# Optimization experiments

Hardware: AMD Instinct MI355X
Metric: run time of the kernel (lower is better)

Reference implementation:

```python
import jax, jax.numpy as jnp
from jax import lax
import numpy as np

B, N, NPOINT, NSAMPLE = 4, 8192, 1024, 32
RADIUS = 0.2
EPS = 1e-5
C_IN = 16
MLP_DIMS = [(3 + C_IN, 64), (64, 64), (64, 128)]


def setup_inputs() -> dict:
    key = jax.random.key(0)
    ks = jax.random.split(key, 16)
    inp = {
        "xyz": jax.random.uniform(ks[0], (B, N, 3), dtype=jnp.float32),
        "points": jax.random.normal(ks[1], (B, N, C_IN), dtype=jnp.float32),
    }
    for i, (cin, cout) in enumerate(MLP_DIMS, 1):
        inp[f"w{i}"] = jax.random.normal(ks[1 + i], (cout, cin), dtype=jnp.float32) / np.sqrt(cin)
        inp[f"b{i}"] = jnp.zeros((cout,), jnp.float32)
        inp[f"g{i}"] = jnp.ones((cout,), jnp.float32)
        inp[f"be{i}"] = jnp.zeros((cout,), jnp.float32)
    return inp


def fps(xyz, npoint):
    # Farthest point sampling; sequential by nature -> lax.scan over npoint steps.
    # Deterministic start at index 0 (torch version uses a random start).
    b, n, _ = xyz.shape
    def step(carry, _):
        dist, far = carry
        centroid = jnp.take_along_axis(xyz, far[:, None, None], axis=1)  # [B,1,3]
        d = jnp.sum((xyz - centroid) ** 2, -1)                            # [B,N]
        dist = jnp.minimum(dist, d)
        return (dist, jnp.argmax(dist, -1).astype(jnp.int32)), far
    init = (jnp.full((b, n), 1e10, xyz.dtype), jnp.zeros((b,), jnp.int32))
    _, idxs = lax.scan(step, init, None, length=npoint)
    return jnp.transpose(idxs)  # [B, npoint]


def gather2(pts, idx):  # pts [B,N,C], idx [B,S] -> [B,S,C]
    return jnp.take_along_axis(pts, idx[..., None], axis=1)


def gather3(pts, idx):  # pts [B,N,C], idx [B,S,K] -> [B,S,K,C]
    b, s, k = idx.shape
    out = jnp.take_along_axis(pts, idx.reshape(b, s * k)[..., None], axis=1)
    return out.reshape(b, s, k, pts.shape[-1])


def ball_query(radius, nsample, xyz, new_xyz):
    n = xyz.shape[1]
    # [B,S,N] pairwise squared distances (the memory-bound hot spot)
    sqr = jnp.sum((new_xyz[:, :, None, :] - xyz[:, None, :, :]) ** 2, -1)
    gidx = jnp.where(sqr > radius * radius, n, jnp.arange(n, dtype=jnp.int32))
    gidx = jnp.sort(gidx, axis=-1)[:, :, :nsample]
    first = gidx[:, :, :1]
    return jnp.where(gidx == n, first, gidx)


def mlp_layer(x, w, b, g, be):
    # 1x1 Conv2d + BatchNorm2d (train mode: batch stats over B,S,K) + ReLU
    y = jnp.einsum('bskc,oc->bsko', x, w) + b
    mu = jnp.mean(y, axis=(0, 1, 2))
    var = jnp.var(y, axis=(0, 1, 2))
    y = (y - mu) * (g * lax.rsqrt(var + EPS)) + be
    return jax.nn.relu(y)


def reference(xyz, points, w1, b1, g1, be1, w2, b2, g2, be2, w3, b3, g3, be3):
    fps_idx = fps(xyz, NPOINT)                       # [B,S]
    new_xyz = gather2(xyz, fps_idx)                  # [B,S,3]
    idx = ball_query(RADIUS, NSAMPLE, xyz, new_xyz)  # [B,S,K]
    grouped_xyz_norm = gather3(xyz, idx) - new_xyz[:, :, None, :]  # [B,S,K,3]
    grouped_points = gather3(points, idx)            # [B,S,K,C]
    feat = jnp.concatenate([grouped_xyz_norm, grouped_points], -1)  # [B,S,K,3+C]
    feat = mlp_layer(feat, w1, b1, g1, be1)
    feat = mlp_layer(feat, w2, b2, g2, be2)
    feat = mlp_layer(feat, w3, b3, g3, be3)
    new_points = jnp.max(feat, axis=2)               # max-pool over neighbors -> [B,S,128]
    return new_xyz, new_points
```

## Files before the change

kernel.cpp:

```cpp
#include <hip/hip_runtime.h>

#define NB 4
#define NP 8192
#define NS 1024
#define NK 32
#define CNT_ALL 131072.0f

typedef float v2f __attribute__((ext_vector_type(2)));
typedef unsigned long long u64;

#define AGENT __HIP_MEMORY_SCOPE_AGENT

template <int CTRL>
__device__ __forceinline__ unsigned dpp_max_u32(unsigned m)
{
    unsigned o = (unsigned)__builtin_amdgcn_update_dpp((int)m, (int)m, CTRL, 0xF, 0xF, false);
    return (o > m) ? o : m;
}

template <int CTRL>
__device__ __forceinline__ u64 dpp_max_u64(u64 k)
{
    unsigned lo = (unsigned)k, hi = (unsigned)(k >> 32);
    unsigned olo = (unsigned)__builtin_amdgcn_update_dpp((int)lo, (int)lo, CTRL, 0xF, 0xF, false);
    unsigned ohi = (unsigned)__builtin_amdgcn_update_dpp((int)hi, (int)hi, CTRL, 0xF, 0xF, false);
    u64 o = ((u64)ohi << 32) | (u64)olo;
    return (o > k) ? o : k;
}

__global__ __launch_bounds__(512, 1) void k1_kernel(
    const float* __restrict__ xyz, const float* __restrict__ pts,
    float* __restrict__ newxyz,
    const float* __restrict__ w1, const float* __restrict__ b1,
    float* __restrict__ y1, float* __restrict__ st, unsigned* __restrict__ prog)
{
    __shared__ __align__(16) char smem[98432];
    const int tid = threadIdx.x;
    const int lane = tid & 63;
    const int wv = tid >> 6;

    if (blockIdx.x < NB) {
#pragma clang fp contract(off)
        float* s_px = (float*)smem;
        float* s_py = (float*)(smem + 32768);
        float* s_pz = (float*)(smem + 65536);
        u64*   s_kv = (u64*)(smem + 98304);
        const int b = blockIdx.x;
        const float* xb = xyz + (size_t)b * NP * 3;

#pragma unroll
        for (int k = 0; k < 16; ++k) {
            const int i = k * 512 + tid;
            s_px[i] = xb[3 * i + 0];
            s_py[i] = xb[3 * i + 1];
            s_pz[i] = xb[3 * i + 2];
        }
        __syncthreads();

        v2f px[8], py[8], pz[8], dist[8];
        const int base = tid << 4;
#pragma unroll
        for (int m = 0; m < 8; ++m) {
            const int p0 = base + 2 * m;
            px[m] = v2f{s_px[p0], s_px[p0 + 1]};
            py[m] = v2f{s_py[p0], s_py[p0 + 1]};
            pz[m] = v2f{s_pz[p0], s_pz[p0 + 1]};
            dist[m] = v2f{1e10f, 1e10f};
        }
        float cx = s_px[0], cy = s_py[0], cz = s_pz[0];
        float* ob = newxyz + (size_t)b * NS * 3;

        for (int it = 0; it < NS; ++it) {
            if (tid == 0) {
                __hip_atomic_store(&prog[b], (unsigned)it, __ATOMIC_RELAXED, AGENT);
                __hip_atomic_store(&ob[it * 3 + 0], cx, __ATOMIC_RELAXED, AGENT);
                __hip_atomic_store(&ob[it * 3 + 1], cy, __ATOMIC_RELAXED, AGENT);
                __hip_atomic_store(&ob[it * 3 + 2], cz, __ATOMIC_RELAXED, AGENT);
            }
            const v2f cxx = v2f{cx, cx}, cyy = v2f{cy, cy}, czz = v2f{cz, cz};
            v2f bdv = v2f{-1.0f, -1.0f};
#pragma unroll
            for (int m = 0; m < 8; ++m) {
                v2f dx = px[m] - cxx, dy = py[m] - cyy, dz = pz[m] - czz;
                v2f d = __builtin_elementwise_fma(dz, dz,
                            __builtin_elementwise_fma(dy, dy, dx * dx));
                v2f dj = __builtin_elementwise_min(dist[m], d);
                dist[m] = dj;
                bdv = __builtin_elementwise_max(bdv, dj);
            }
            const float bd = fmaxf(bdv.x, bdv.y);
            const unsigned ub = __float_as_uint(bd);
            unsigned m0 = dpp_max_u32<0xB1>(ub);
            m0 = dpp_max_u32<0x4E>(m0);
            m0 = dpp_max_u32<0x141>(m0);
            m0 = dpp_max_u32<0x140>(m0);
            m0 = dpp_max_u32<0x142>(m0);
            m0 = dpp_max_u32<0x143>(m0);
            const unsigned maxbits = (unsigned)__builtin_amdgcn_readlane((int)m0, 63);
            const float bdw = __uint_as_float(maxbits);
            int jb = 0;
#pragma unroll
            for (int m = 7; m >= 0; --m) {
                jb = (dist[m].y == bdw) ? (2 * m + 1) : jb;
                jb = (dist[m].x == bdw) ? (2 * m) : jb;
            }
            const u64 bm = __ballot(ub == maxbits);
            const int srclane = __ffsll(bm) - 1;
            const int wbi = __builtin_amdgcn_readlane(base + jb, srclane);
            if (lane == 0)
                s_kv[(it & 1) * 8 + wv] = ((u64)maxbits << 32) | (unsigned)(NP - 1 - wbi);
            __syncthreads();
            u64 kv = s_kv[(it & 1) * 8 + (lane & 7)];
            kv = dpp_max_u64<0xB1>(kv);
            kv = dpp_max_u64<0x4E>(kv);
            kv = dpp_max_u64<0x141>(kv);
            const int fi = NP - 1 - (int)(unsigned)(kv & 0xFFFFFFFFull);
            cx = s_px[fi]; cy = s_py[fi]; cz = s_pz[fi];
        }
        if (tid == 0)
            __hip_atomic_store(&prog[b], (unsigned)NS, __ATOMIC_RELAXED, AGENT);
        return;
    }

    int*   s_ball = (int*)smem;
    float* s_cent = (float*)(smem + 1024);
    float* s_feat = (float*)(smem + 1152);
    float* s_ps   = (float*)(smem + 1152 + 20480);
    float* s_pq   = s_ps + 512;

    const int abk = blockIdx.x - NB;
    const int b = abk >> 5;
    const int s0 = (abk & 31) * 32;
    const float* xb = xyz + (size_t)b * NP * 3;
    const float rr = (float)(0.2 * 0.2);

    const int c = tid & 63, rg = tid >> 6;
    float wvr[20];
#pragma unroll
    for (int j = 0; j < 19; ++j) wvr[j] = w1[c * 19 + j];
    wvr[19] = 0.f;
    const float bs = b1[c];
    float sa = 0.f, qa = 0.f;

    for (int chunk = 0; chunk < 4; ++chunk) {
        const int sl = s0 + chunk * 8;
        if (tid == 0) {
            while ((int)__hip_atomic_load(&prog[b], __ATOMIC_RELAXED, AGENT) < sl + 8)
                __builtin_amdgcn_s_sleep(4);
        }
        __syncthreads();
        {
            const int sg = (b << 10) + sl + wv;
            float cxv, cyv, czv;
            if (lane == 0) {
                cxv = __hip_atomic_load(&newxyz[sg * 3 + 0], __ATOMIC_RELAXED, AGENT);
                cyv = __hip_atomic_load(&newxyz[sg * 3 + 1], __ATOMIC_RELAXED, AGENT);
                czv = __hip_atomic_load(&newxyz[sg * 3 + 2], __ATOMIC_RELAXED, AGENT);
                s_cent[wv * 4 + 0] = cxv;
                s_cent[wv * 4 + 1] = cyv;
                s_cent[wv * 4 + 2] = czv;
            }
            cxv = __shfl(cxv, 0); cyv = __shfl(cyv, 0); czv = __shfl(czv, 0);
            int cnt = 0;
            for (int bse = 0; bse < NP && cnt < NK; bse += 64) {
                const int p = bse + lane;
                float dx = xb[p * 3 + 0] - cxv;
                float dy = xb[p * 3 + 1] - cyv;
                float dz = xb[p * 3 + 2] - czv;
                float d = __fadd_rn(__fadd_rn(__fmul_rn(dx, dx), __fmul_rn(dy, dy)),
                                    __fmul_rn(dz, dz));
                bool in = (d <= rr);
                u64 mask = __ballot(in);
                int before = __popcll(mask & ((1ull << lane) - 1ull));
                int pos = cnt + before;
                if (in && pos < NK) s_ball[wv * NK + pos] = p;
                cnt += (int)__popcll(mask);
            }
            cnt = min(cnt, NK);
            const int v0 = s_ball[wv * NK];
            if (lane < NK && lane >= cnt) s_ball[wv * NK + lane] = v0;
        }
        __syncthreads();
        if (tid < 256) {
            const int lg = tid >> 5, k = tid & 31;
            const int id = s_ball[lg * NK + k];
            const float* pp = xyz + ((size_t)b * NP + id) * 3;
            float* f = s_feat + tid * 20;
            f[0] = pp[0] - s_cent[lg * 4 + 0];
            f[1] = pp[1] - s_cent[lg * 4 + 1];
            f[2] = pp[2] - s_cent[lg * 4 + 2];
            const float4* q4 = (const float4*)(pts + ((size_t)b * NP + id) * 16);
#pragma unroll
            for (int i = 0; i < 4; ++i) {
                float4 v = q4[i];
                f[3 + 4 * i + 0] = v.x; f[3 + 4 * i + 1] = v.y;
                f[3 + 4 * i + 2] = v.z; f[3 + 4 * i + 3] = v.w;
            }
            f[19] = 0.f;
        }
        __syncthreads();
        const size_t rowbase = (size_t)abk * 1024 + (size_t)chunk * 256;
        for (int r = 0; r < 32; ++r) {
            const int row = rg * 32 + r;
            const float4* f4 = (const float4*)(s_feat + row * 20);
            float acc = bs;
#pragma unroll
            for (int j4 = 0; j4 < 5; ++j4) {
                float4 v = f4[j4];
                acc += wvr[4*j4+0]*v.x + wvr[4*j4+1]*v.y + wvr[4*j4+2]*v.z + wvr[4*j4+3]*v.w;
            }
            y1[(rowbase + row) * 64 + c] = acc;
            sa += acc; qa += acc * acc;
        }
        __syncthreads();
    }
    s_ps[tid] = sa; s_pq[tid] = qa;
    __syncthreads();
    if (tid < 64) {
        float ts = 0.f, tq = 0.f;
#pragma unroll
        for (int i = 0; i < 8; ++i) { ts += s_ps[i * 64 + tid]; tq += s_pq[i * 64 + tid]; }
        atomicAdd(&st[(abk & 7) * 64 + tid], ts);
        atomicAdd(&st[512 + (abk & 7) * 64 + tid], tq);
    }
}

__device__ __forceinline__ void bn_coef(const float* __restrict__ sums,
                                        const float* __restrict__ sqs,
                                        const float* __restrict__ g,
                                        const float* __restrict__ be,
                                        int C, int c, float& sc, float& sh)
{
    float s = 0.f, q = 0.f;
#pragma unroll
    for (int k = 0; k < 8; ++k) { s += sums[k * C + c]; q += sqs[k * C + c]; }
    const float mean = s / CNT_ALL;
    const float var = q / CNT_ALL - mean * mean;
    sc = g[c] / sqrtf(var + 1e-5f);
    sh = be[c] - mean * sc;
}

__global__ __launch_bounds__(256) void phaseB_kernel(
    const float* __restrict__ y1,
    const float* __restrict__ g1, const float* __restrict__ be1,
    const float* __restrict__ w2, const float* __restrict__ b2,
    float* __restrict__ y2, float* __restrict__ st)
{
    __shared__ float x_lds[128 * 64];
    __shared__ float s_sc[64], s_sh[64];
    __shared__ float s_ps[256], s_pq[256];
    const float* sums1 = st;
    const float* sqs1 = st + 512;
    float* sums2 = st + 1024;
    float* sqs2 = st + 1536;

    const int tid = threadIdx.x;
    const int bk = blockIdx.x;
    if (tid < 64) {
        float sc, sh;
        bn_coef(sums1, sqs1, g1, be1, 64, tid, sc, sh);
        s_sc[tid] = sc; s_sh[tid] = sh;
    }
    __syncthreads();
    const int c = tid & 63, rg = tid >> 6;
    float wv[64];
#pragma unroll
    for (int j = 0; j < 64; ++j) wv[j] = w2[c * 64 + j];
    const float bs = b2[c];
    float s = 0.f, q = 0.f;
    for (int half = 0; half < 2; ++half) {
        const size_t row0 = (size_t)256 * bk + 128 * half;
        const float4* y1g = (const float4*)(y1 + row0 * 64);
        float4* xl4 = (float4*)x_lds;
#pragma unroll
        for (int i = 0; i < 8; ++i) {
            const int slot = i * 256 + tid;
            float4 v = y1g[slot];
            const int c4 = (slot & 15) * 4;
            float4 o;
            o.x = fmaxf(v.x * s_sc[c4+0] + s_sh[c4+0], 0.f);
            o.y = fmaxf(v.y * s_sc[c4+1] + s_sh[c4+1], 0.f);
            o.z = fmaxf(v.z * s_sc[c4+2] + s_sh[c4+2], 0.f);
            o.w = fmaxf(v.w * s_sc[c4+3] + s_sh[c4+3], 0.f);
            xl4[slot] = o;
        }
        __syncthreads();
        for (int r = 0; r < 32; ++r) {
            const int row = rg * 32 + r;
            const float4* x4 = (const float4*)(x_lds + row * 64);
            float acc = bs;
#pragma unroll
            for (int j4 = 0; j4 < 16; ++j4) {
                float4 v = x4[j4];
                acc += wv[4*j4+0]*v.x + wv[4*j4+1]*v.y + wv[4*j4+2]*v.z + wv[4*j4+3]*v.w;
            }
            y2[(row0 + row) * 64 + c] = acc;
            s += acc; q += acc * acc;
        }
        __syncthreads();
    }
    s_ps[tid] = s; s_pq[tid] = q;
    __syncthreads();
    if (rg == 0) {
        float ts = s_ps[c] + s_ps[64 + c] + s_ps[128 + c] + s_ps[192 + c];
        float tq = s_pq[c] + s_pq[64 + c] + s_pq[128 + c] + s_pq[192 + c];
        atomicAdd(&sums2[(bk & 7) * 64 + c], ts);
        atomicAdd(&sqs2[(bk & 7) * 64 + c], tq);
    }
}

__global__ __launch_bounds__(256) void phaseC2_kernel(
    const float* __restrict__ y2,
    const float* __restrict__ g2, const float* __restrict__ be2,
    const float* __restrict__ w3, const float* __restrict__ b3,
    float* __restrict__ st, float* __restrict__ mxb, float* __restrict__ mnb)
{
    __shared__ float s_x[NK * 64];
    __shared__ float s_sc[64], s_sh[64];
    __shared__ float s_p3s[256], s_p3q[256];
    __shared__ float s_mx[256], s_mn[256];
    const float* sums2 = st + 1024;
    const float* sqs2 = st + 1536;
    float* sums3 = st + 2048;
    float* sqs3 = st + 3072;

    const int tid = threadIdx.x;
    const int bk = blockIdx.x;
    if (tid < 64) {
        float sc, sh;
        bn_coef(sums2, sqs2, g2, be2, 64, tid, sc, sh);
        s_sc[tid] = sc; s_sh[tid] = sh;
    }
    __syncthreads();
    const int c = tid & 127, rg = tid >> 7;
    float wv[64];
#pragma unroll
    for (int j = 0; j < 64; ++j) wv[j] = w3[c * 64 + j];
    const float bs = b3[c];
    float s = 0.f, q = 0.f;
    for (int gi = 0; gi < 8; ++gi) {
        const size_t grow0 = (size_t)256 * bk + 32 * gi;
        const float4* y2g = (const float4*)(y2 + grow0 * 64);
        float4* sx4 = (float4*)s_x;
#pragma unroll
        for (int i = 0; i < 2; ++i) {
            const int slot = i * 256 + tid;
            float4 v = y2g[slot];
            const int c4 = (slot & 15) * 4;
            float4 o;
            o.x = fmaxf(v.x * s_sc[c4+0] + s_sh[c4+0], 0.f);
            o.y = fmaxf(v.y * s_sc[c4+1] + s_sh[c4+1], 0.f);
            o.z = fmaxf(v.z * s_sc[c4+2] + s_sh[c4+2], 0.f);
            o.w = fmaxf(v.w * s_sc[c4+3] + s_sh[c4+3], 0.f);
            sx4[slot] = o;
        }
        __syncthreads();
        float mx = -1e30f, mn = 1e30f;
        for (int r = 0; r < 16; ++r) {
            const int row = rg * 16 + r;
            const float4* x4 = (const float4*)(s_x + row * 64);
            float acc = bs;
#pragma unroll
            for (int j4 = 0; j4 < 16; ++j4) {
                float4 v = x4[j4];
                acc += wv[4*j4+0]*v.x + wv[4*j4+1]*v.y + wv[4*j4+2]*v.z + wv[4*j4+3]*v.w;
            }
            s += acc; q += acc * acc;
            mx = fmaxf(mx, acc); mn = fminf(mn, acc);
        }
        s_mx[rg * 128 + c] = mx; s_mn[rg * 128 + c] = mn;
        __syncthreads();
        if (rg == 0) {
            const size_t gidx = (size_t)(8 * bk + gi) * 128 + c;
            mxb[gidx] = fmaxf(s_mx[c], s_mx[128 + c]);
            mnb[gidx] = fminf(s_mn[c], s_mn[128 + c]);
        }
        __syncthreads();
    }
    s_p3s[rg * 128 + c] = s; s_p3q[rg * 128 + c] = q;
    __syncthreads();
    if (rg == 0) {
        atomicAdd(&sums3[(bk & 7) * 128 + c], s_p3s[c] + s_p3s[128 + c]);
        atomicAdd(&sqs3[(bk & 7) * 128 + c], s_p3q[c] + s_p3q[128 + c]);
    }
}

__global__ __launch_bounds__(256) void phaseD2_kernel(
    const float* __restrict__ st,
    const float* __restrict__ g3, const float* __restrict__ be3,
    const float* __restrict__ mxb, const float* __restrict__ mnb,
    float* __restrict__ out_np)
{
    const int idx = blockIdx.x * 256 + threadIdx.x;
    const int c = idx & 127;
    float sc, sh;
    bn_coef(st + 2048, st + 3072, g3, be3, 128, c, sc, sh);
    const float sel = (sc >= 0.f) ? mxb[idx] : mnb[idx];
    out_np[idx] = fmaxf(sel * sc + sh, 0.f);
}

extern "C" void kernel_launch(void* const* d_in, const int* in_sizes, int n_in,
                              void* d_out, int out_size, void* d_ws, size_t ws_size,
                              hipStream_t stream)
{
    (void)in_sizes; (void)n_in; (void)out_size;
    const float* xyz = (const float*)d_in[0];
    const float* pts = (const float*)d_in[1];
    const float* w1 = (const float*)d_in[2];
    const float* b1 = (const float*)d_in[3];
    const float* g1 = (const float*)d_in[4];
    const float* be1 = (const float*)d_in[5];
    const float* w2 = (const float*)d_in[6];
    const float* b2 = (const float*)d_in[7];
    const float* g2 = (const float*)d_in[8];
    const float* be2 = (const float*)d_in[9];
    const float* w3 = (const float*)d_in[10];
    const float* b3 = (const float*)d_in[11];
    const float* g3 = (const float*)d_in[12];
    const float* be3 = (const float*)d_in[13];

    float* out = (float*)d_out;
    float* newxyz = out;
    float* newpts = out + NB * NS * 3;

    float* y1 = (float*)d_ws;
    float* y2 = y1 + 8388608;
    float* st = y2 + 8388608;
    unsigned* prog = (unsigned*)(st + 4096);
    float* mxb = st + 4104;
    float* mnb = mxb + 524288;
    const size_t needed = (2ull * 8388608ull + 4104ull + 2ull * 524288ull) * 4ull;
    if (ws_size < needed) return;

    hipMemsetAsync(st, 0, (4096 + 8) * sizeof(float), stream);
    k1_kernel<<<NB + 128, 512, 0, stream>>>(xyz, pts, newxyz, w1, b1, y1, st, prog);
    phaseB_kernel<<<512, 256, 0, stream>>>(y1, g1, be1, w2, b2, y2, st);
    phaseC2_kernel<<<512, 256, 0, stream>>>(y2, g2, be2, w3, b3, st, mxb, mnb);
    phaseD2_kernel<<<2048, 256, 0, stream>>>(st, g3, be3, mxb, mnb, newpts);
}
```

Baseline: 1.002 ms.

## Sort FPS points by Morton cell and skip distant point groups via bounding spheres

The farthest-point-sampling block now bins points into an 8x8x8 Morton grid, counting-sorts them into shared memory, and assigns each wave four spatially coherent groups of 256 points with per-group bounding spheres. Each iteration skips the distance update for a group when the new centroid is too far to lower any distance in it, using a triangle-inequality threshold built from the group's current max distance. The argmax is packed into a single 64-bit key of distance, original index and slot. This is meant to cut the per-iteration ALU work on the serial FPS critical path. In exchange it adds sort setup, more shared memory, a wave-uniform branch and a different reduction, and the tie-breaking and float-threshold margins must still reproduce the reference selection exactly.

```diff
diff --git a/kernel.cpp b/kernel.cpp
--- a/kernel.cpp
+++ b/kernel.cpp
@@ -6,26 +6,59 @@
 #define NK 32
 #define CNT_ALL 131072.0f
 
-typedef float v2f __attribute__((ext_vector_type(2)));
 typedef unsigned long long u64;
+typedef unsigned u32;
 
 #define AGENT __HIP_MEMORY_SCOPE_AGENT
 
 template <int CTRL>
-__device__ __forceinline__ unsigned dpp_max_u32(unsigned m)
-{
-    unsigned o = (unsigned)__builtin_amdgcn_update_dpp((int)m, (int)m, CTRL, 0xF, 0xF, false);
+__device__ __forceinline__ u32 dpp_max_u32(u32 m)
+{
+    u32 o = (u32)__builtin_amdgcn_update_dpp((int)m, (int)m, CTRL, 0xF, 0xF, false);
     return (o > m) ? o : m;
 }
-
+template <int CTRL>
+__device__ __forceinline__ u32 dpp_min_u32(u32 m)
+{
+    u32 o = (u32)__builtin_amdgcn_update_dpp((int)m, (int)m, CTRL, 0xF, 0xF, false);
+    return (o < m) ? o : m;
+}
 template <int CTRL>
 __device__ __forceinline__ u64 dpp_max_u64(u64 k)
 {
-    unsigned lo = (unsigned)k, hi = (unsigned)(k >> 32);
-    unsigned olo = (unsigned)__builtin_amdgcn_update_dpp((int)lo, (int)lo, CTRL, 0xF, 0xF, false);
-    unsigned ohi = (unsigned)__builtin_amdgcn_update_dpp((int)hi, (int)hi, CTRL, 0xF, 0xF, false);
+    u32 lo = (u32)k, hi = (u32)(k >> 32);
+    u32 olo = (u32)__builtin_amdgcn_update_dpp((int)lo, (int)lo, CTRL, 0xF, 0xF, false);
+    u32 ohi = (u32)__builtin_amdgcn_update_dpp((int)hi, (int)hi, CTRL, 0xF, 0xF, false);
     u64 o = ((u64)ohi << 32) | (u64)olo;
     return (o > k) ? o : k;
+}
+__device__ __forceinline__ u32 wave_max_u32(u32 m)
+{
+    m = dpp_max_u32<0xB1>(m);  m = dpp_max_u32<0x4E>(m);
+    m = dpp_max_u32<0x141>(m); m = dpp_max_u32<0x140>(m);
+    m = dpp_max_u32<0x142>(m); m = dpp_max_u32<0x143>(m);
+    return (u32)__builtin_amdgcn_readlane((int)m, 63);
+}
+__device__ __forceinline__ u32 wave_min_u32(u32 m)
+{
+    m = dpp_min_u32<0xB1>(m);  m = dpp_min_u32<0x4E>(m);
+    m = dpp_min_u32<0x141>(m); m = dpp_min_u32<0x140>(m);
+    m = dpp_min_u32<0x142>(m); m = dpp_min_u32<0x143>(m);
+    return (u32)__builtin_amdgcn_readlane((int)m, 63);
+}
+__device__ __forceinline__ u64 wave_max_u64(u64 k)
+{
+    k = dpp_max_u64<0xB1>(k);  k = dpp_max_u64<0x4E>(k);
+    k = dpp_max_u64<0x141>(k); k = dpp_max_u64<0x140>(k);
+    k = dpp_max_u64<0x142>(k); k = dpp_max_u64<0x143>(k);
+    u32 lo = (u32)__builtin_amdgcn_readlane((int)(u32)k, 63);
+    u32 hi = (u32)__builtin_amdgcn_readlane((int)(u32)(k >> 32), 63);
+    return ((u64)hi << 32) | lo;
+}
+
+__device__ __forceinline__ u32 expand3(u32 v)
+{
+    return (v & 1u) | ((v & 2u) << 2) | ((v & 4u) << 4);
 }
 
 __global__ __launch_bounds__(512, 1) void k1_kernel(
@@ -34,17 +67,20 @@
     const float* __restrict__ w1, const float* __restrict__ b1,
     float* __restrict__ y1, float* __restrict__ st, unsigned* __restrict__ prog)
 {
-    __shared__ __align__(16) char smem[98432];
+    __shared__ __align__(16) char smem[135296];
     const int tid = threadIdx.x;
     const int lane = tid & 63;
     const int wv = tid >> 6;
 
     if (blockIdx.x < NB) {
 #pragma clang fp contract(off)
-        float* s_px = (float*)smem;
-        float* s_py = (float*)(smem + 32768);
-        float* s_pz = (float*)(smem + 65536);
-        u64*   s_kv = (u64*)(smem + 98304);
+        float* s_px   = (float*)smem;
+        float* s_py   = (float*)(smem + 32768);
+        float* s_pz   = (float*)(smem + 65536);
+        u32*   s_sidx = (u32*)(smem + 98304);
+        u32*   s_hist = (u32*)(smem + 131072);
+        u32*   s_scan = (u32*)(smem + 133120);
+        u64*   s_kv   = (u64*)(smem + 135168);
         const int b = blockIdx.x;
         const float* xb = xyz + (size_t)b * NP * 3;
 
@@ -55,19 +91,105 @@
             s_py[i] = xb[3 * i + 1];
             s_pz[i] = xb[3 * i + 2];
         }
-        __syncthreads();
-
-        v2f px[8], py[8], pz[8], dist[8];
-        const int base = tid << 4;
-#pragma unroll
-        for (int m = 0; m < 8; ++m) {
-            const int p0 = base + 2 * m;
-            px[m] = v2f{s_px[p0], s_px[p0 + 1]};
-            py[m] = v2f{s_py[p0], s_py[p0 + 1]};
-            pz[m] = v2f{s_pz[p0], s_pz[p0 + 1]};
-            dist[m] = v2f{1e10f, 1e10f};
-        }
-        float cx = s_px[0], cy = s_py[0], cz = s_pz[0];
+        s_hist[tid] = 0;
+        __syncthreads();
+
+#pragma unroll
+        for (int k = 0; k < 16; ++k) {
+            const int i = k * 512 + tid;
+            const u32 ix = min((u32)(s_px[i] * 8.f), 7u);
+            const u32 iy = min((u32)(s_py[i] * 8.f), 7u);
+            const u32 iz = min((u32)(s_pz[i] * 8.f), 7u);
+            const u32 cell = (expand3(ix) << 2) | (expand3(iy) << 1) | expand3(iz);
+            atomicAdd(&s_hist[cell], 1u);
+        }
+        __syncthreads();
+        {
+            const u32 own = s_hist[tid];
+            u32 run = own;
+            s_scan[tid] = run;
+            __syncthreads();
+            for (int off = 1; off < 512; off <<= 1) {
+                const u32 add = (tid >= off) ? s_scan[tid - off] : 0u;
+                __syncthreads();
+                run += add;
+                s_scan[tid] = run;
+                __syncthreads();
+            }
+            s_scan[tid] = run - own;
+        }
+        __syncthreads();
+#pragma unroll
+        for (int k = 0; k < 16; ++k) {
+            const int i = k * 512 + tid;
+            const u32 ix = min((u32)(s_px[i] * 8.f), 7u);
+            const u32 iy = min((u32)(s_py[i] * 8.f), 7u);
+            const u32 iz = min((u32)(s_pz[i] * 8.f), 7u);
+            const u32 cell = (expand3(ix) << 2) | (expand3(iy) << 1) | expand3(iz);
+            const u32 slot = atomicAdd(&s_scan[cell], 1u);
+            s_sidx[slot] = (u32)i;
+        }
+        __syncthreads();
+
+        float px[4][4], py[4][4], pz[4][4], dist[4][4];
+        u32 lowkey[4][4];
+#pragma unroll
+        for (int q = 0; q < 4; ++q) {
+#pragma unroll
+            for (int j = 0; j < 4; ++j) {
+                const int slot = 1024 * wv + 256 * q + 4 * lane + j;
+                const u32 oi = s_sidx[slot];
+                px[q][j] = s_px[oi];
+                py[q][j] = s_py[oi];
+                pz[q][j] = s_pz[oi];
+                dist[q][j] = 1e10f;
+                lowkey[q][j] = ((8191u - oi) << 13) | (u32)slot;
+            }
+        }
+        __syncthreads();
+#pragma unroll
+        for (int q = 0; q < 4; ++q) {
+#pragma unroll
+            for (int j = 0; j < 4; ++j) {
+                const int slot = 1024 * wv + 256 * q + 4 * lane + j;
+                s_px[slot] = px[q][j];
+                s_py[slot] = py[q][j];
+                s_pz[slot] = pz[q][j];
+            }
+        }
+        __syncthreads();
+
+        float cmx[4], cmy[4], cmz[4], thrbase[4], thr[4];
+        u64 K[4] = {0, 0, 0, 0};
+#pragma unroll
+        for (int q = 0; q < 4; ++q) {
+            float mnx = px[q][0], mxx = px[q][0];
+            float mny = py[q][0], mxy = py[q][0];
+            float mnz = pz[q][0], mxz = pz[q][0];
+#pragma unroll
+            for (int j = 1; j < 4; ++j) {
+                mnx = fminf(mnx, px[q][j]); mxx = fmaxf(mxx, px[q][j]);
+                mny = fminf(mny, py[q][j]); mxy = fmaxf(mxy, py[q][j]);
+                mnz = fminf(mnz, pz[q][j]); mxz = fmaxf(mxz, pz[q][j]);
+            }
+            mnx = __uint_as_float(wave_min_u32(__float_as_uint(mnx)));
+            mxx = __uint_as_float(wave_max_u32(__float_as_uint(mxx)));
+            mny = __uint_as_float(wave_min_u32(__float_as_uint(mny)));
+            mxy = __uint_as_float(wave_max_u32(__float_as_uint(mxy)));
+            mnz = __uint_as_float(wave_min_u32(__float_as_uint(mnz)));
+            mxz = __uint_as_float(wave_max_u32(__float_as_uint(mxz)));
+            cmx[q] = (mnx + mxx) * 0.5f;
+            cmy[q] = (mny + mxy) * 0.5f;
+            cmz[q] = (mnz + mxz) * 0.5f;
+            const float hx = (mxx - mnx) * 0.5f;
+            const float hy = (mxy - mny) * 0.5f;
+            const float hz = (mxz - mnz) * 0.5f;
+            const float rb = sqrtf(hx * hx + hy * hy + hz * hz) * 1.000002f + 1e-7f;
+            thrbase[q] = rb + 1e-5f;
+            thr[q] = thrbase[q] + 1e5f;
+        }
+
+        float cx = xb[0], cy = xb[1], cz = xb[2];
         float* ob = newxyz + (size_t)b * NS * 3;
 
         for (int it = 0; it < NS; ++it) {
@@ -77,45 +199,49 @@
                 __hip_atomic_store(&ob[it * 3 + 1], cy, __ATOMIC_RELAXED, AGENT);
                 __hip_atomic_store(&ob[it * 3 + 2], cz, __ATOMIC_RELAXED, AGENT);
             }
-            const v2f cxx = v2f{cx, cx}, cyy = v2f{cy, cy}, czz = v2f{cz, cz};
-            v2f bdv = v2f{-1.0f, -1.0f};
-#pragma unroll
-            for (int m = 0; m < 8; ++m) {
-                v2f dx = px[m] - cxx, dy = py[m] - cyy, dz = pz[m] - czz;
-                v2f d = __builtin_elementwise_fma(dz, dz,
-                            __builtin_elementwise_fma(dy, dy, dx * dx));
-                v2f dj = __builtin_elementwise_min(dist[m], d);
-                dist[m] = dj;
-                bdv = __builtin_elementwise_max(bdv, dj);
-            }
-            const float bd = fmaxf(bdv.x, bdv.y);
-            const unsigned ub = __float_as_uint(bd);
-            unsigned m0 = dpp_max_u32<0xB1>(ub);
-            m0 = dpp_max_u32<0x4E>(m0);
-            m0 = dpp_max_u32<0x141>(m0);
-            m0 = dpp_max_u32<0x140>(m0);
-            m0 = dpp_max_u32<0x142>(m0);
-            m0 = dpp_max_u32<0x143>(m0);
-            const unsigned maxbits = (unsigned)__builtin_amdgcn_readlane((int)m0, 63);
-            const float bdw = __uint_as_float(maxbits);
-            int jb = 0;
-#pragma unroll
-            for (int m = 7; m >= 0; --m) {
-                jb = (dist[m].y == bdw) ? (2 * m + 1) : jb;
-                jb = (dist[m].x == bdw) ? (2 * m) : jb;
-            }
-            const u64 bm = __ballot(ub == maxbits);
-            const int srclane = __ffsll(bm) - 1;
-            const int wbi = __builtin_amdgcn_readlane(base + jb, srclane);
-            if (lane == 0)
-                s_kv[(it & 1) * 8 + wv] = ((u64)maxbits << 32) | (unsigned)(NP - 1 - wbi);
+#pragma unroll
+            for (int q = 0; q < 4; ++q) {
+                const float tdx = cx - cmx[q], tdy = cy - cmy[q], tdz = cz - cmz[q];
+                const float t2 = fmaf(tdz, tdz, fmaf(tdy, tdy, tdx * tdx));
+                const bool need = (t2 < thr[q] * thr[q]);
+                if (__builtin_amdgcn_readfirstlane((int)need)) {
+                    float mloc = -1.f;
+#pragma unroll
+                    for (int j = 0; j < 4; ++j) {
+                        const float dx = px[q][j] - cx;
+                        const float dy = py[q][j] - cy;
+                        const float dz = pz[q][j] - cz;
+                        const float d = fmaf(dz, dz, fmaf(dy, dy, dx * dx));
+                        const float dj = fminf(dist[q][j], d);
+                        dist[q][j] = dj;
+                        mloc = fmaxf(mloc, dj);
+                    }
+                    u64 kk = 0;
+#pragma unroll
+                    for (int j = 0; j < 4; ++j) {
+                        const u64 cand = ((u64)__float_as_uint(dist[q][j]) << 26)
+                                       | lowkey[q][j];
+                        kk = (cand > kk) ? cand : kk;
+                    }
+                    K[q] = kk;
+                    const u32 mbits = wave_max_u32(__float_as_uint(mloc));
+                    const float sm = sqrtf(__uint_as_float(mbits)) * 1.000001f + 1e-7f;
+                    thr[q] = thrbase[q] + sm;
+                }
+            }
+            u64 lk = K[0];
+            lk = (K[1] > lk) ? K[1] : lk;
+            lk = (K[2] > lk) ? K[2] : lk;
+            lk = (K[3] > lk) ? K[3] : lk;
+            const u64 wk = wave_max_u64(lk);
+            if (lane == 0) s_kv[(it & 1) * 8 + wv] = wk;
             __syncthreads();
             u64 kv = s_kv[(it & 1) * 8 + (lane & 7)];
             kv = dpp_max_u64<0xB1>(kv);
             kv = dpp_max_u64<0x4E>(kv);
             kv = dpp_max_u64<0x141>(kv);
-            const int fi = NP - 1 - (int)(unsigned)(kv & 0xFFFFFFFFull);
-            cx = s_px[fi]; cy = s_py[fi]; cz = s_pz[fi];
+            const int fs = (int)(kv & 0x1FFFull);
+            cx = s_px[fs]; cy = s_py[fs]; cz = s_pz[fs];
         }
         if (tid == 0)
             __hip_atomic_store(&prog[b], (unsigned)NS, __ATOMIC_RELAXED, AGENT);
```

Result: slower. 1.809 ms (+80.6%).
